# Performance work log

Hardware: AMD Instinct MI355X
Metric: run time of the kernel (lower is better)

Reference implementation:

```python
import jax, jax.numpy as jnp
import numpy as np

PATCH_SIZE = 16


def setup_inputs() -> dict:
    key = jax.random.key(0)
    images = jax.random.normal(key, (64, 384, 384, 3), dtype=jnp.float32)
    return {"images": images}


def reference(images) -> jnp.ndarray:
    # images: [B, H, W, 3], channels-last. Extract non-overlapping PxP patches
    # and flatten each (row-major over (P, P, 3), matching torch.flatten).
    b, h, w, c = images.shape
    p = PATCH_SIZE
    g = h // p  # grid size
    # [B, G, P, G, P, C] -> [B, G, G, P, P, C] -> [B, G*G, P*P*C]
    x = images.reshape(b, g, p, g, p, c)
    x = x.transpose(0, 1, 3, 2, 4, 5)
    return x.reshape(b, g * g, p * p * c)
```

## Files before the change

kernel.cpp:

```cpp
#include <hip/hip_runtime.h>


typedef float f4 __attribute__((ext_vector_type(4)));

constexpr int C     = 3;
constexpr int P     = 16;
constexpr int G     = 24;
constexpr int ROW4  = 384 * C / 4;
constexpr int IMG4  = 384 * ROW4;
constexpr int HR    = 8;
constexpr int TILE4 = HR * ROW4;
constexpr int LSTR  = ROW4 + 1;
constexpr int BLOCK = 256;
constexpr int PT    = TILE4 / BLOCK;
constexpr int NSLAB = 64 * G * 2;
constexpr int GRID  = 1024;
constexpr int NITER = NSLAB / GRID;

constexpr int GY4   = G * P * P * C / 4;
constexpr int HALF4 = HR * P * C / 4;

__device__ __forceinline__ int in_base_of(int s) {
    int half = s & 1, bg = s >> 1;
    int gy = bg % G, b = bg / G;
    return b * IMG4 + (gy * P + half * HR) * ROW4;
}
__device__ __forceinline__ int out_base_of(int s) {
    int half = s & 1, bg = s >> 1;
    int gy = bg % G, b = bg / G;
    return b * IMG4 + gy * GY4 + half * HALF4;
}

__global__ __launch_bounds__(BLOCK, 4)
void patches_kernel(const f4* __restrict__ in, f4* __restrict__ out) {
    __shared__ f4 lds[HR * LSTR];
    const int t  = threadIdx.x;
    const int s0 = blockIdx.x;

    f4 v[PT], u[PT];
    {
        const f4* p = in + in_base_of(s0) + t;
#pragma unroll
        for (int j = 0; j < PT; ++j)
            v[j] = p[j * BLOCK];
    }

#pragma unroll
    for (int i = 0; i < NITER; ++i) {
        if (i + 1 < NITER) {
            const f4* p = in + in_base_of(s0 + (i + 1) * GRID) + t;
#pragma unroll
            for (int j = 0; j < PT; ++j)
                u[j] = p[j * BLOCK];
            __builtin_amdgcn_sched_barrier(0);
        }

        if (i > 0)
            __builtin_amdgcn_s_barrier();

#pragma unroll
        for (int j = 0; j < PT; ++j) {
            int idx = t + j * BLOCK;
            int row = idx / ROW4;
            int col = idx - row * ROW4;
            lds[row * LSTR + col] = v[j];
        }
        asm volatile("s_waitcnt lgkmcnt(0)" ::: "memory");
        __builtin_amdgcn_s_barrier();

        const int ob = out_base_of(s0 + i * GRID);
#pragma unroll
        for (int j = 0; j < PT; ++j) {
            int o  = t + j * BLOCK;
            int gx = o / 96;
            int w  = o - gx * 96;
            int py = w / 12;
            int k  = w - py * 12;
            out[ob + gx * 192 + w] = lds[py * LSTR + gx * 12 + k];
        }

        if (i + 1 < NITER) {
#pragma unroll
            for (int j = 0; j < PT; ++j) v[j] = u[j];
        }
    }
}

extern "C" void kernel_launch(void* const* d_in, const int* in_sizes, int n_in,
                              void* d_out, int out_size, void* d_ws, size_t ws_size,
                              hipStream_t stream) {
    const f4* in  = (const f4*)d_in[0];
    f4*       out = (f4*)d_out;
    patches_kernel<<<GRID, BLOCK, 0, stream>>>(in, out);
}
```

Before: 197.2 us.

## Give each wave its own two-row tile to drop block barriers, use nontemporal memory ops

Splits work so each 64-lane wave owns a two-row slice of a patch row and transposes it through a private LDS region. This removes the workgroup-wide s_barrier calls, leaving only a per-wave lgkmcnt wait. Loads and stores become nontemporal to avoid polluting caches on this single-pass copy. The trade-off is smaller per-wave tiles, which give shorter contiguous output runs (24 f4 per patch row instead of 96).

```diff
diff --git a/kernel.cpp b/kernel.cpp
--- a/kernel.cpp
+++ b/kernel.cpp
@@ -3,80 +3,75 @@
 
 typedef float f4 __attribute__((ext_vector_type(4)));
 
-constexpr int C     = 3;
-constexpr int P     = 16;
-constexpr int G     = 24;
-constexpr int ROW4  = 384 * C / 4;
+constexpr int ROW4  = 288;
 constexpr int IMG4  = 384 * ROW4;
-constexpr int HR    = 8;
-constexpr int TILE4 = HR * ROW4;
-constexpr int LSTR  = ROW4 + 1;
+constexpr int GY4   = 24 * 192;
+constexpr int LROW  = ROW4 + 1;
+constexpr int LWAVE = 2 * LROW;
 constexpr int BLOCK = 256;
-constexpr int PT    = TILE4 / BLOCK;
-constexpr int NSLAB = 64 * G * 2;
 constexpr int GRID  = 1024;
-constexpr int NITER = NSLAB / GRID;
+constexpr int NW    = GRID * 4;
+constexpr int NTILE = 64 * 24 * 8;
+constexpr int NITER = NTILE / NW;
+constexpr int PT    = 9;
 
-constexpr int GY4   = G * P * P * C / 4;
-constexpr int HALF4 = HR * P * C / 4;
-
-__device__ __forceinline__ int in_base_of(int s) {
-    int half = s & 1, bg = s >> 1;
-    int gy = bg % G, b = bg / G;
-    return b * IMG4 + (gy * P + half * HR) * ROW4;
+__device__ __forceinline__ int in_base_of(int tau) {
+    int p = tau & 7, t2 = tau >> 3;
+    int gy = t2 % 24, b = t2 / 24;
+    return b * IMG4 + (gy * 16 + 2 * p) * ROW4;
 }
-__device__ __forceinline__ int out_base_of(int s) {
-    int half = s & 1, bg = s >> 1;
-    int gy = bg % G, b = bg / G;
-    return b * IMG4 + gy * GY4 + half * HALF4;
+__device__ __forceinline__ int out_base_of(int tau) {
+    int p = tau & 7, t2 = tau >> 3;
+    int gy = t2 % 24, b = t2 / 24;
+    return b * IMG4 + gy * GY4 + p * 24;
 }
 
 __global__ __launch_bounds__(BLOCK, 4)
 void patches_kernel(const f4* __restrict__ in, f4* __restrict__ out) {
-    __shared__ f4 lds[HR * LSTR];
-    const int t  = threadIdx.x;
-    const int s0 = blockIdx.x;
+    __shared__ f4 lds[4 * LWAVE];
+    const int wv = threadIdx.x >> 6;
+    const int l  = threadIdx.x & 63;
+    f4* __restrict__ L = &lds[wv * LWAVE];
+    const int W = blockIdx.x * 4 + wv;
 
     f4 v[PT], u[PT];
     {
-        const f4* p = in + in_base_of(s0) + t;
+        const f4* p = in + in_base_of(W) + l;
 #pragma unroll
         for (int j = 0; j < PT; ++j)
-            v[j] = p[j * BLOCK];
+            v[j] = __builtin_nontemporal_load(p + j * 64);
     }
 
 #pragma unroll
     for (int i = 0; i < NITER; ++i) {
         if (i + 1 < NITER) {
-            const f4* p = in + in_base_of(s0 + (i + 1) * GRID) + t;
+            const f4* p = in + in_base_of(W + (i + 1) * NW) + l;
 #pragma unroll
             for (int j = 0; j < PT; ++j)
-                u[j] = p[j * BLOCK];
+                u[j] = __builtin_nontemporal_load(p + j * 64);
             __builtin_amdgcn_sched_barrier(0);
         }
 
-        if (i > 0)
-            __builtin_amdgcn_s_barrier();
-
 #pragma unroll
         for (int j = 0; j < PT; ++j) {
-            int idx = t + j * BLOCK;
-            int row = idx / ROW4;
-            int col = idx - row * ROW4;
-            lds[row * LSTR + col] = v[j];
+            int idx = l + j * 64;
+            int r   = idx / ROW4;
+            int c   = idx - r * ROW4;
+            L[r * LROW + c] = v[j];
         }
         asm volatile("s_waitcnt lgkmcnt(0)" ::: "memory");
-        __builtin_amdgcn_s_barrier();
+        __builtin_amdgcn_sched_barrier(0);
 
-        const int ob = out_base_of(s0 + i * GRID);
+        const int ob = out_base_of(W + i * NW);
 #pragma unroll
         for (int j = 0; j < PT; ++j) {
-            int o  = t + j * BLOCK;
-            int gx = o / 96;
-            int w  = o - gx * 96;
-            int py = w / 12;
-            int k  = w - py * 12;
-            out[ob + gx * 192 + w] = lds[py * LSTR + gx * 12 + k];
+            int o   = l + j * 64;
+            int gx  = o / 24;
+            int w2  = o - gx * 24;
+            int py2 = w2 / 12;
+            int k   = w2 - py2 * 12;
+            f4 x = L[py2 * LROW + gx * 12 + k];
+            __builtin_nontemporal_store(x, out + ob + gx * 192 + w2);
         }
 
         if (i + 1 < NITER) {
```

New measurement: 185.8 us. 1.06x faster.
